# Optimization experiments

Hardware: AMD Instinct MI355X
Metric: run time of the kernel (lower is better)

The kernel has to match this reference:

```python
import jax, jax.numpy as jnp
import numpy as np

B, S, D = 512, 199, 128
PRO, SKILL = 20000, 500


def setup_inputs() -> dict:
    key = jax.random.key(0)
    ks = jax.random.split(key, 32)
    rn = lambda k, shape: jax.random.normal(k, shape, dtype=jnp.float32) * 0.05
    inp = {}
    inp["last_problem"] = jax.random.randint(ks[0], (B, S), 0, PRO, dtype=jnp.int32)
    inp["last_skill"] = jax.random.randint(ks[1], (B, S), 0, SKILL, dtype=jnp.int32)
    inp["last_ans"] = jax.random.randint(ks[2], (B, S), 0, 2, dtype=jnp.int32)
    inp["next_problem"] = jax.random.randint(ks[3], (B, S), 0, PRO, dtype=jnp.int32)
    inp["next_skill"] = jax.random.randint(ks[4], (B, S), 0, SKILL, dtype=jnp.int32)
    inp["next_ans"] = jax.random.randint(ks[5], (B, S), 0, 2, dtype=jnp.int32)
    inp["pro_embed"] = rn(ks[6], (PRO, D))
    inp["skill_embed"] = rn(ks[7], (SKILL, D))
    inp["ans_embed"] = rn(ks[8], (2, D))
    inp["time_embed"] = rn(ks[9], (200, D))
    inp["ls_state"] = rn(ks[10], (1, D))
    inp["pro_state0"] = rn(ks[11], (199, D))
    inp["skill_state0"] = rn(ks[12], (199, D))
    inp["akt_pro_diff"] = rn(ks[13], (PRO, 1))
    inp["akt_pro_change"] = rn(ks[14], (SKILL, D))
    # Linear weights stored as [in, out] (torch W.T); biases zero-init.
    inp["W_pf"] = rn(ks[15], (2 * D, D)); inp["b_pf"] = jnp.zeros((D,), jnp.float32)
    inp["W_sf"] = rn(ks[16], (2 * D, D)); inp["b_sf"] = jnp.zeros((D,), jnp.float32)
    inp["W_af"] = rn(ks[17], (2 * D, D)); inp["b_af"] = jnp.zeros((D,), jnp.float32)
    inp["W_ps"] = rn(ks[18], (2 * D, D)); inp["b_ps"] = jnp.zeros((D,), jnp.float32)
    inp["W_ss"] = rn(ks[19], (2 * D, D)); inp["b_ss"] = jnp.zeros((D,), jnp.float32)
    inp["W_as"] = rn(ks[20], (2 * D, D)); inp["b_as"] = jnp.zeros((D,), jnp.float32)
    inp["W_o1"] = rn(ks[21], (4 * D, D)); inp["b_o1"] = jnp.zeros((D,), jnp.float32)
    inp["W_o2"] = rn(ks[22], (D, 1));     inp["b_o2"] = jnp.zeros((1,), jnp.float32)
    return inp


def _forward(next_problem, next_skill, next_ans,
             pro_embed, skill_embed, ans_embed, time_embed, ls_state,
             pro_state0, skill_state0, akt_pro_diff, akt_pro_change,
             W_pf, b_pf, W_sf, b_sf, W_af, b_af,
             W_ps, b_ps, W_ss, b_ss, W_as, b_as,
             W_o1, b_o1, W_o2, b_o2):
    Bb, Ss = next_problem.shape
    Dd = pro_embed.shape[1]
    # [B,S,D] question embedding with AKT-style difficulty modulation
    npe = (pro_embed[next_problem] + skill_embed[next_skill]
           + akt_pro_diff[next_problem] * akt_pro_change[next_skill])
    nX = npe + ans_embed[next_ans]
    atge = time_embed[1]  # all_time_gap == 1 every step
    bidx = jnp.arange(Bb)

    def step(carry, x):
        pro_state, skill_state, all_state, lpt_tab, lst_tab = carry
        t, npe_t, nX_t, pidx, sidx = x
        # gather last-seen states via per-batch time indices
        lpt = lpt_tab[bidx, pidx]               # [B] int
        lbp = pro_state[bidx, lpt]              # [B,D]
        tge = time_embed[t - lpt]               # [B,D]
        lst = lst_tab[bidx, sidx]
        lbs = skill_state[bidx, lst]
        stge = time_embed[t - lst]
        # forget gates
        lbp = lbp * jax.nn.sigmoid(jnp.concatenate([lbp, tge], -1) @ W_pf + b_pf)
        lbs = lbs * jax.nn.sigmoid(jnp.concatenate([lbs, stge], -1) @ W_sf + b_sf)
        atge_b = jnp.broadcast_to(atge, all_state.shape)
        la = all_state * jax.nn.sigmoid(jnp.concatenate([all_state, atge_b], -1) @ W_af + b_af)
        # prediction head
        final = jnp.concatenate([la, lbp, lbs, npe_t], -1)  # [B,4D]
        P = jax.nn.sigmoid(jax.nn.relu(final @ W_o1 + b_o1) @ W_o2 + b_o2)[:, 0]
        # state updates
        new_all = la + jnp.tanh(jnp.concatenate([la, nX_t], -1) @ W_as + b_as)
        new_pro = lbp + jnp.tanh(jnp.concatenate([lbp, nX_t], -1) @ W_ps + b_ps)
        new_skill = lbs + jnp.tanh(jnp.concatenate([lbs, nX_t], -1) @ W_ss + b_ss)
        # scatter time and state back
        lpt_tab = lpt_tab.at[bidx, pidx].set(t)
        lst_tab = lst_tab.at[bidx, sidx].set(t)
        pro_state = jax.lax.dynamic_update_slice_in_dim(pro_state, new_pro[:, None, :], t, axis=1)
        skill_state = jax.lax.dynamic_update_slice_in_dim(skill_state, new_skill[:, None, :], t, axis=1)
        return (pro_state, skill_state, new_all, lpt_tab, lst_tab), P

    init = (jnp.broadcast_to(pro_state0[None], (Bb, pro_state0.shape[0], Dd)),
            jnp.broadcast_to(skill_state0[None], (Bb, skill_state0.shape[0], Dd)),
            jnp.broadcast_to(ls_state, (Bb, Dd)),
            jnp.zeros((Bb, akt_pro_diff.shape[0]), jnp.int32),
            jnp.zeros((Bb, akt_pro_change.shape[0]), jnp.int32))
    xs = (jnp.arange(Ss, dtype=jnp.int32),
          jnp.swapaxes(npe, 0, 1), jnp.swapaxes(nX, 0, 1),
          next_problem.T, next_skill.T)
    _, Ps = jax.lax.scan(step, init, xs)  # Ps: [S,B]
    return Ps.T  # [B,S]


def reference(last_problem, last_skill, last_ans, next_problem, next_skill, next_ans,
              pro_embed, skill_embed, ans_embed, time_embed, ls_state,
              pro_state0, skill_state0, akt_pro_diff, akt_pro_change,
              W_pf, b_pf, W_sf, b_sf, W_af, b_af,
              W_ps, b_ps, W_ss, b_ss, W_as, b_as,
              W_o1, b_o1, W_o2, b_o2):
    # last_problem/last_skill/last_ans are only used for shape in the original forward
    return _forward(next_problem, next_skill, next_ans,
                    pro_embed, skill_embed, ans_embed, time_embed, ls_state,
                    pro_state0, skill_state0, akt_pro_diff, akt_pro_change,
                    W_pf, b_pf, W_sf, b_sf, W_af, b_af,
                    W_ps, b_ps, W_ss, b_ss, W_as, b_as,
                    W_o1, b_o1, W_o2, b_o2)
```

## Files before the change

kernel.cpp:

```cpp
#include <hip/hip_runtime.h>
#include <hip/hip_bf16.h>

typedef __bf16 bf16;
typedef bf16 bf16x8 __attribute__((ext_vector_type(8)));
typedef bf16 bf16x4 __attribute__((ext_vector_type(4)));
typedef float f32x4 __attribute__((ext_vector_type(4)));
typedef unsigned int u32;
typedef unsigned short u16;

#define Bsz 512
#define Ssz 199
#define Dsz 128
#define GR 16
#define NBLK (Bsz / GR)
#define BTot (Bsz * Ssz)

__device__ __forceinline__ float fsig(float x) {
  return __builtin_amdgcn_rcpf(1.f + __builtin_amdgcn_exp2f(x * -1.44269504f));
}
__device__ __forceinline__ float ftanh(float x) {
  return 1.f - 2.f * __builtin_amdgcn_rcpf(1.f + __builtin_amdgcn_exp2f(x * 2.88539008f));
}
__device__ __forceinline__ f32x4 mfma16(bf16x8 a, bf16x8 b, f32x4 c) {
  return __builtin_amdgcn_mfma_f32_16x16x32_bf16(a, b, c, 0, 0, 0);
}
__device__ __forceinline__ bf16x8 ldfrag(const bf16* PW, int KS, int nt, int ks, int lane) {
  return *(const bf16x8*)&PW[(size_t)((nt * KS + ks) * 64 + lane) * 8];
}
__device__ __forceinline__ void keep(bf16x8& v) {
  f32x4& f = reinterpret_cast<f32x4&>(v);
  asm volatile("" : "+v"(f));
}
__device__ __forceinline__ void barL() {
  __builtin_amdgcn_sched_barrier(0);
  asm volatile("s_waitcnt lgkmcnt(0)" ::: "memory");
  __builtin_amdgcn_s_barrier();
  __builtin_amdgcn_sched_barrier(0);
}

__global__ void k_idx(const int* __restrict__ np_, const int* __restrict__ ns_,
                      const int* __restrict__ na_, u32* __restrict__ idx) {
  __shared__ u16 tabP[20000];
  __shared__ u16 tabS[500];
  __shared__ u16 pb[Ssz], sb[Ssz];
  __shared__ unsigned char ab[Ssz];
  int b = blockIdx.x;
  for (int i = threadIdx.x; i < 20000; i += blockDim.x) tabP[i] = 0;
  for (int i = threadIdx.x; i < 500; i += blockDim.x) tabS[i] = 0;
  for (int i = threadIdx.x; i < Ssz; i += blockDim.x) {
    pb[i] = (u16)np_[b * Ssz + i];
    sb[i] = (u16)ns_[b * Ssz + i];
    ab[i] = (unsigned char)na_[b * Ssz + i];
  }
  __syncthreads();
  if (threadIdx.x == 0) {
    for (int t = 0; t < Ssz; ++t) {
      int p = pb[t], s = sb[t];
      idx[b * Ssz + t] = (u32)tabP[p] | ((u32)tabS[s] << 8) | ((u32)ab[t] << 16);
      tabP[p] = (u16)t;
      tabS[s] = (u16)t;
    }
  }
}

__global__ void k_pack(const float* __restrict__ W, bf16* __restrict__ dst, int K) {
  int g = blockIdx.x * blockDim.x + threadIdx.x;
  int KS = K / 32;
  int total = 8 * KS * 64;
  if (g >= total) return;
  int l = g & 63;
  int ks = (g >> 6) % KS;
  int nt = (g >> 6) / KS;
  int col = nt * 16 + (l & 15);
  int k0 = ks * 32 + (l >> 4) * 8;
  bf16x8 v;
  for (int j = 0; j < 8; ++j) v[j] = (bf16)W[(size_t)(k0 + j) * 128 + col];
  *(bf16x8*)&dst[(size_t)g * 8] = v;
}

__global__ void k_tge(const float* __restrict__ TE, const float* __restrict__ W,
                      const float* __restrict__ bias, float* __restrict__ dst) {
  __shared__ float te[128];
  int d = blockIdx.x, n = threadIdx.x;
  te[n] = TE[d * 128 + n];
  __syncthreads();
  float acc = bias[n];
  for (int k = 0; k < 128; ++k) acc += te[k] * W[(size_t)(128 + k) * 128 + n];
  dst[d * 128 + n] = acc;
}

__global__ void k_embed(const int* __restrict__ np_, const int* __restrict__ ns_,
                        const float* __restrict__ pe, const float* __restrict__ se,
                        const float* __restrict__ diff, const float* __restrict__ chg,
                        bf16* __restrict__ npe) {
  int g = blockIdx.x * 256 + threadIdx.x;
  int bt = g >> 5, cg = (g & 31) * 4;
  if (bt >= BTot) return;
  int p = np_[bt], s = ns_[bt];
  float d = diff[p];
  f32x4 a = *(const f32x4*)&pe[(size_t)p * 128 + cg];
  f32x4 b = *(const f32x4*)&se[(size_t)s * 128 + cg];
  f32x4 c = *(const f32x4*)&chg[(size_t)s * 128 + cg];
  bf16x4 v;
  for (int j = 0; j < 4; ++j) v[j] = (bf16)(a[j] + b[j] + d * c[j]);
  *(bf16x4*)&npe[(size_t)bt * 128 + cg] = v;
}

struct MainParams {
  const int *next_problem, *next_skill;
  const float *pro_embed, *skill_embed, *akt_pro_diff, *akt_pro_change;
  const float *ans_embed;
  const float *ls_state, *pro_state0, *skill_state0;
  const u32 *idx;
  const bf16 *npe;
  const float *TGEp, *TGEs, *cAF;
  const bf16 *PWpf, *PWsf, *PWaf, *PWps, *PWss, *PWas;
  const float *b_ps, *b_ss, *b_as;
  bf16 *proSt, *skSt, *Sla, *Slbp, *Slbs;
};

template <int EMB>
__global__ void __launch_bounds__(512, 1) k_main(MainParams P) {
  const int b0 = blockIdx.x * GR;
  const int tid = threadIdx.x;
  const int lane = tid & 63;
  const int wv = tid >> 6;
  const int r32 = tid >> 5;
  const int c4 = (tid & 31) * 4;
  const int arow = lane & 15, apos = (lane >> 4) * 8;
  const int rb = (lane >> 4) * 4;
  const int cA = wv * 16 + (lane & 15);

  __shared__ __align__(16) bf16 Ala[16][136], Albp[16][136], Albs[16][136], AnX[16][136];
  __shared__ __align__(16) bf16 STG0[16][132], STG1[16][132], STGa[16][132];
  __shared__ u32 idxL[GR * Ssz];

  bf16x8 Wpf[4], Wsf[4], Waf[4], Wps[8], Wss[8], Was[8];
#pragma unroll
  for (int ks = 0; ks < 4; ++ks) {
    Wpf[ks] = ldfrag(P.PWpf, 4, wv, ks, lane);
    Wsf[ks] = ldfrag(P.PWsf, 4, wv, ks, lane);
    Waf[ks] = ldfrag(P.PWaf, 4, wv, ks, lane);
  }
#pragma unroll
  for (int ks = 0; ks < 8; ++ks) {
    Wps[ks] = ldfrag(P.PWps, 8, wv, ks, lane);
    Wss[ks] = ldfrag(P.PWss, 8, wv, ks, lane);
    Was[ks] = ldfrag(P.PWas, 8, wv, ks, lane);
  }
#pragma unroll
  for (int ks = 0; ks < 4; ++ks) {
    keep(Wpf[ks]);
    keep(Wsf[ks]);
    keep(Waf[ks]);
  }
#pragma unroll
  for (int ks = 0; ks < 8; ++ks) {
    keep(Wps[ks]);
    keep(Wss[ks]);
    keep(Was[ks]);
  }
  const float bpsv = P.b_ps[cA], bssv = P.b_ss[cA], basv = P.b_as[cA], cafv = P.cAF[cA];
  float aeL[4], aeH[4];
#pragma unroll
  for (int j = 0; j < 4; ++j) {
    aeL[j] = P.ans_embed[c4 + j];
    aeH[j] = P.ans_embed[128 + c4 + j];
  }

  for (int i = tid; i < GR * Ssz; i += 512) idxL[i] = P.idx[b0 * Ssz + i];
  __syncthreads();

  float gpc[4], gsc[4];
  {
    bf16x4 va, vp, vs;
    for (int j = 0; j < 4; ++j) {
      va[j] = (bf16)P.ls_state[c4 + j];
      vp[j] = (bf16)P.pro_state0[c4 + j];
      vs[j] = (bf16)P.skill_state0[c4 + j];
    }
    *(bf16x4*)&Ala[r32][c4] = va;
    *(bf16x4*)&Albp[r32][c4] = vp;
    *(bf16x4*)&Albs[r32][c4] = vs;
    u32 iw0 = idxL[r32 * Ssz];
    int na0 = (iw0 >> 16) & 1;
    f32x4 np0;
    if (EMB) {
      bf16x4 nb = *(const bf16x4*)&P.npe[((size_t)(b0 + r32) * Ssz) * Dsz + c4];
      for (int j = 0; j < 4; ++j) np0[j] = (float)nb[j];
    } else {
      int bt = (b0 + r32) * Ssz;
      int np = P.next_problem[bt], ns = P.next_skill[bt];
      float d = P.akt_pro_diff[np];
      f32x4 a = *(const f32x4*)&P.pro_embed[(size_t)np * 128 + c4];
      f32x4 b = *(const f32x4*)&P.skill_embed[(size_t)ns * 128 + c4];
      f32x4 c = *(const f32x4*)&P.akt_pro_change[(size_t)ns * 128 + c4];
      for (int j = 0; j < 4; ++j) np0[j] = a[j] + b[j] + d * c[j];
    }
    bf16x4 vx;
    for (int j = 0; j < 4; ++j) vx[j] = (bf16)(np0[j] + (na0 ? aeH[j] : aeL[j]));
    *(bf16x4*)&AnX[r32][c4] = vx;
#pragma unroll
    for (int r = 0; r < 4; ++r) {
      gpc[r] = P.TGEp[cA];
      gsc[r] = P.TGEs[cA];
    }
  }
  __syncthreads();

  for (int t = 0; t < Ssz; ++t) {
    const bool pf = (t + 1 < Ssz);
    float gpn[4], gsn[4];
    bf16x4 pPro{}, pSk{}, pNp{};
    f32x4 pNpF{};
    u32 iwN = 0;
    if (pf) {
#pragma unroll
      for (int r = 0; r < 4; ++r) {
        u32 iw = idxL[(rb + r) * Ssz + t + 1];
        int lp = iw & 255, ls = (iw >> 8) & 255;
        gpn[r] = P.TGEp[(size_t)(t + 1 - lp) * Dsz + cA];
        gsn[r] = P.TGEs[(size_t)(t + 1 - ls) * Dsz + cA];
      }
      iwN = idxL[r32 * Ssz + t + 1];
      int lpN = iwN & 255, lsN = (iwN >> 8) & 255;
      if (lpN != t)
        pPro = *(const bf16x4*)&P.proSt[((size_t)(b0 + r32) * Ssz + lpN) * Dsz + c4];
      if (lsN != t)
        pSk = *(const bf16x4*)&P.skSt[((size_t)(b0 + r32) * Ssz + lsN) * Dsz + c4];
      if (EMB) {
        pNp = *(const bf16x4*)&P.npe[((size_t)(b0 + r32) * Ssz + t + 1) * Dsz + c4];
      } else {
        int bt = (b0 + r32) * Ssz + t + 1;
        int np = P.next_problem[bt], ns = P.next_skill[bt];
        float d = P.akt_pro_diff[np];
        f32x4 a = *(const f32x4*)&P.pro_embed[(size_t)np * 128 + c4];
        f32x4 b = *(const f32x4*)&P.skill_embed[(size_t)ns * 128 + c4];
        f32x4 c = *(const f32x4*)&P.akt_pro_change[(size_t)ns * 128 + c4];
        for (int j = 0; j < 4; ++j) pNpF[j] = a[j] + b[j] + d * c[j];
      }
    }
    f32x4 dpf{}, dsf{}, daf{};
#pragma unroll
    for (int ks = 0; ks < 4; ++ks) {
      bf16x8 ap = *(const bf16x8*)&Albp[arow][ks * 32 + apos];
      bf16x8 av = *(const bf16x8*)&Albs[arow][ks * 32 + apos];
      bf16x8 aa = *(const bf16x8*)&Ala[arow][ks * 32 + apos];
      dpf = mfma16(ap, Wpf[ks], dpf);
      dsf = mfma16(av, Wsf[ks], dsf);
      daf = mfma16(aa, Waf[ks], daf);
    }
    barL();
    float gP[4], gS[4], gA[4];
#pragma unroll
    for (int r = 0; r < 4; ++r) {
      int row = rb + r;
      float sp = (float)Albp[row][cA];
      float gv = sp * fsig(dpf[r] + gpc[r]);
      gP[r] = gv;
      Albp[row][cA] = (bf16)gv;
      float ss = (float)Albs[row][cA];
      float gw = ss * fsig(dsf[r] + gsc[r]);
      gS[r] = gw;
      Albs[row][cA] = (bf16)gw;
      float sa = (float)Ala[row][cA];
      float gx = sa * fsig(daf[r] + cafv);
      gA[r] = gx;
      Ala[row][cA] = (bf16)gx;
    }
    barL();
    f32x4 uas{}, ups{}, uss{};
#pragma unroll
    for (int ks = 0; ks < 4; ++ks) {
      bf16x8 aa = *(const bf16x8*)&Ala[arow][ks * 32 + apos];
      bf16x8 ap = *(const bf16x8*)&Albp[arow][ks * 32 + apos];
      bf16x8 av = *(const bf16x8*)&Albs[arow][ks * 32 + apos];
      bf16x8 ax = *(const bf16x8*)&AnX[arow][ks * 32 + apos];
      uas = mfma16(aa, Was[ks], uas);
      uas = mfma16(ax, Was[ks + 4], uas);
      ups = mfma16(ap, Wps[ks], ups);
      ups = mfma16(ax, Wps[ks + 4], ups);
      uss = mfma16(av, Wss[ks], uss);
      uss = mfma16(ax, Wss[ks + 4], uss);
    }
#pragma unroll
    for (int r = 0; r < 4; ++r) {
      int row = rb + r;
      STG0[row][cA] = (bf16)(gP[r] + ftanh(ups[r] + bpsv));
      STG1[row][cA] = (bf16)(gS[r] + ftanh(uss[r] + bssv));
      STGa[row][cA] = (bf16)(gA[r] + ftanh(uas[r] + basv));
    }
    barL();
    {
      size_t base = ((size_t)(b0 + r32) * Ssz + t) * Dsz + c4;
      *(bf16x4*)&P.Sla[base] = *(const bf16x4*)&Ala[r32][c4];
      *(bf16x4*)&P.Slbp[base] = *(const bf16x4*)&Albp[r32][c4];
      *(bf16x4*)&P.Slbs[base] = *(const bf16x4*)&Albs[r32][c4];
      bf16x4 npv = *(const bf16x4*)&STG0[r32][c4];
      bf16x4 nsv = *(const bf16x4*)&STG1[r32][c4];
      *(bf16x4*)&P.proSt[base] = npv;
      *(bf16x4*)&P.skSt[base] = nsv;
      if (pf) {
        int lpN = iwN & 255, lsN = (iwN >> 8) & 255, naN = (iwN >> 16) & 1;
        *(bf16x4*)&Ala[r32][c4] = *(const bf16x4*)&STGa[r32][c4];
        *(bf16x4*)&Albp[r32][c4] = (lpN == t) ? npv : pPro;
        *(bf16x4*)&Albs[r32][c4] = (lsN == t) ? nsv : pSk;
        bf16x4 vx;
        for (int j = 0; j < 4; ++j) {
          float f = EMB ? (float)pNp[j] : pNpF[j];
          vx[j] = (bf16)(f + (naN ? aeH[j] : aeL[j]));
        }
        *(bf16x4*)&AnX[r32][c4] = vx;
#pragma unroll
        for (int r = 0; r < 4; ++r) {
          gpc[r] = gpn[r];
          gsc[r] = gsn[r];
        }
      }
    }
    __syncthreads();
  }
}

struct HeadParams {
  const bf16 *Sla, *Slbp, *Slbs, *PWo1, *npe;
  const int *next_problem, *next_skill;
  const float *pro_embed, *skill_embed, *akt_pro_diff, *akt_pro_change;
  const float *b_o1, *W_o2, *b_o2;
  float *out;
};

template <int EMB>
__global__ void k_head(HeadParams P) {
  const int bt0 = blockIdx.x * 16;
  const int tid = threadIdx.x, lane = tid & 63, wv = tid >> 6;
  const int r16 = tid >> 4, c8 = (tid & 15) * 8;
  const int arow = lane & 15, apos = (lane >> 4) * 8;
  const int rb = (lane >> 4) * 4;
  const int nt0 = wv, nt1 = wv + 4;
  const int cAh = nt0 * 16 + (lane & 15), cBh = nt1 * 16 + (lane & 15);
  __shared__ __align__(16) bf16 Af[16][520];
  __shared__ float Hh[16][132];
  __shared__ float Hpart[16][16];
  __shared__ float w2s[128];
  if (tid < 128) w2s[tid] = P.W_o2[tid];
  {
    int bt = bt0 + r16;
    *(bf16x8*)&Af[r16][c8] = *(const bf16x8*)&P.Sla[(size_t)bt * 128 + c8];
    *(bf16x8*)&Af[r16][128 + c8] = *(const bf16x8*)&P.Slbp[(size_t)bt * 128 + c8];
    *(bf16x8*)&Af[r16][256 + c8] = *(const bf16x8*)&P.Slbs[(size_t)bt * 128 + c8];
    if (EMB) {
      *(bf16x8*)&Af[r16][384 + c8] = *(const bf16x8*)&P.npe[(size_t)bt * 128 + c8];
    } else {
      int np = P.next_problem[bt], ns = P.next_skill[bt];
      float diff = P.akt_pro_diff[np];
      f32x4 p0 = *(const f32x4*)&P.pro_embed[(size_t)np * 128 + c8];
      f32x4 p1 = *(const f32x4*)&P.pro_embed[(size_t)np * 128 + c8 + 4];
      f32x4 s0 = *(const f32x4*)&P.skill_embed[(size_t)ns * 128 + c8];
      f32x4 s1 = *(const f32x4*)&P.skill_embed[(size_t)ns * 128 + c8 + 4];
      f32x4 c0 = *(const f32x4*)&P.akt_pro_change[(size_t)ns * 128 + c8];
      f32x4 c1 = *(const f32x4*)&P.akt_pro_change[(size_t)ns * 128 + c8 + 4];
      bf16x8 vn;
      for (int j = 0; j < 4; ++j) {
        vn[j] = (bf16)(p0[j] + s0[j] + diff * c0[j]);
        vn[j + 4] = (bf16)(p1[j] + s1[j] + diff * c1[j]);
      }
      *(bf16x8*)&Af[r16][384 + c8] = vn;
    }
  }
  __syncthreads();
  f32x4 h0{}, h1{};
#pragma unroll
  for (int ks = 0; ks < 16; ++ks) {
    bf16x8 a = *(const bf16x8*)&Af[arow][ks * 32 + apos];
    h0 = mfma16(a, ldfrag(P.PWo1, 16, nt0, ks, lane), h0);
    h1 = mfma16(a, ldfrag(P.PWo1, 16, nt1, ks, lane), h1);
  }
  const float bo1A = P.b_o1[cAh], bo1B = P.b_o1[cBh];
  for (int r = 0; r < 4; ++r) {
    Hh[rb + r][cAh] = fmaxf(h0[r] + bo1A, 0.f);
    Hh[rb + r][cBh] = fmaxf(h1[r] + bo1B, 0.f);
  }
  __syncthreads();
  {
    int row = tid >> 4, cg = tid & 15;
    float s = 0.f;
    for (int j = 0; j < 8; ++j) s += Hh[row][cg * 8 + j] * w2s[cg * 8 + j];
    Hpart[row][cg] = s;
  }
  __syncthreads();
  if (tid < 16) {
    float s = 0.f;
    for (int k = 0; k < 16; ++k) s += Hpart[tid][k];
    P.out[bt0 + tid] = fsig(s + P.b_o2[0]);
  }
}

extern "C" void kernel_launch(void* const* d_in, const int* in_sizes, int n_in,
                              void* d_out, int out_size, void* d_ws, size_t ws_size,
                              hipStream_t stream) {
  const int* next_problem = (const int*)d_in[3];
  const int* next_skill = (const int*)d_in[4];
  const int* next_ans = (const int*)d_in[5];
  const float* pro_embed = (const float*)d_in[6];
  const float* skill_embed = (const float*)d_in[7];
  const float* ans_embed = (const float*)d_in[8];
  const float* time_embed = (const float*)d_in[9];
  const float* ls_state = (const float*)d_in[10];
  const float* pro_state0 = (const float*)d_in[11];
  const float* skill_state0 = (const float*)d_in[12];
  const float* akt_pro_diff = (const float*)d_in[13];
  const float* akt_pro_change = (const float*)d_in[14];
  const float* W_pf = (const float*)d_in[15];
  const float* b_pf = (const float*)d_in[16];
  const float* W_sf = (const float*)d_in[17];
  const float* b_sf = (const float*)d_in[18];
  const float* W_af = (const float*)d_in[19];
  const float* b_af = (const float*)d_in[20];
  const float* W_ps = (const float*)d_in[21];
  const float* b_ps = (const float*)d_in[22];
  const float* W_ss = (const float*)d_in[23];
  const float* b_ss = (const float*)d_in[24];
  const float* W_as = (const float*)d_in[25];
  const float* b_as = (const float*)d_in[26];
  const float* W_o1 = (const float*)d_in[27];
  const float* b_o1 = (const float*)d_in[28];
  const float* W_o2 = (const float*)d_in[29];
  const float* b_o2 = (const float*)d_in[30];

  char* ws = (char*)d_ws;
  size_t off = 0;
  auto alloc = [&](size_t bytes) -> void* {
    void* p = ws + off;
    off += bytes;
    off = (off + 255) & ~(size_t)255;
    return p;
  };
  bf16* proSt = (bf16*)alloc((size_t)Bsz * Ssz * Dsz * 2);
  bf16* skSt = (bf16*)alloc((size_t)Bsz * Ssz * Dsz * 2);
  u32* idx = (u32*)alloc((size_t)BTot * 4);
  float* TGEp = (float*)alloc(200 * 128 * 4);
  float* TGEs = (float*)alloc(200 * 128 * 4);
  float* cAF = (float*)alloc(128 * 4);
  bf16* PWpf = (bf16*)alloc(128 * 128 * 2);
  bf16* PWsf = (bf16*)alloc(128 * 128 * 2);
  bf16* PWaf = (bf16*)alloc(128 * 128 * 2);
  bf16* PWps = (bf16*)alloc(256 * 128 * 2);
  bf16* PWss = (bf16*)alloc(256 * 128 * 2);
  bf16* PWas = (bf16*)alloc(256 * 128 * 2);
  bf16* PWo1 = (bf16*)alloc(512 * 128 * 2);
  bf16* Sla = (bf16*)alloc((size_t)BTot * Dsz * 2);
  bf16* Slbp = (bf16*)alloc((size_t)BTot * Dsz * 2);
  bf16* Slbs = (bf16*)alloc((size_t)BTot * Dsz * 2);
  size_t off_base = off;
  bf16* npe = (bf16*)alloc((size_t)BTot * Dsz * 2);
  size_t off_emb = off;

  bool emb = (off_emb <= ws_size);
  if (!emb && off_base > ws_size) {
    hipMemsetAsync(d_out, 0xFF, (size_t)out_size * 4, stream);
    return;
  }

  k_idx<<<Bsz, 256, 0, stream>>>(next_problem, next_skill, next_ans, idx);
  k_pack<<<8, 256, 0, stream>>>(W_pf, PWpf, 128);
  k_pack<<<8, 256, 0, stream>>>(W_sf, PWsf, 128);
  k_pack<<<8, 256, 0, stream>>>(W_af, PWaf, 128);
  k_pack<<<16, 256, 0, stream>>>(W_ps, PWps, 256);
  k_pack<<<16, 256, 0, stream>>>(W_ss, PWss, 256);
  k_pack<<<16, 256, 0, stream>>>(W_as, PWas, 256);
  k_pack<<<32, 256, 0, stream>>>(W_o1, PWo1, 512);
  k_tge<<<200, 128, 0, stream>>>(time_embed, W_pf, b_pf, TGEp);
  k_tge<<<200, 128, 0, stream>>>(time_embed, W_sf, b_sf, TGEs);
  k_tge<<<1, 128, 0, stream>>>(time_embed + 128, W_af, b_af, cAF);
  if (emb)
    k_embed<<<(BTot * 32 + 255) / 256, 256, 0, stream>>>(
        next_problem, next_skill, pro_embed, skill_embed, akt_pro_diff, akt_pro_change, npe);

  MainParams mp;
  mp.next_problem = next_problem; mp.next_skill = next_skill;
  mp.pro_embed = pro_embed; mp.skill_embed = skill_embed;
  mp.akt_pro_diff = akt_pro_diff; mp.akt_pro_change = akt_pro_change;
  mp.ans_embed = ans_embed;
  mp.ls_state = ls_state; mp.pro_state0 = pro_state0; mp.skill_state0 = skill_state0;
  mp.idx = idx; mp.npe = npe;
  mp.TGEp = TGEp; mp.TGEs = TGEs; mp.cAF = cAF;
  mp.PWpf = PWpf; mp.PWsf = PWsf; mp.PWaf = PWaf;
  mp.PWps = PWps; mp.PWss = PWss; mp.PWas = PWas;
  mp.b_ps = b_ps; mp.b_ss = b_ss; mp.b_as = b_as;
  mp.proSt = proSt; mp.skSt = skSt;
  mp.Sla = Sla; mp.Slbp = Slbp; mp.Slbs = Slbs;

  HeadParams hp;
  hp.Sla = Sla; hp.Slbp = Slbp; hp.Slbs = Slbs; hp.PWo1 = PWo1; hp.npe = npe;
  hp.next_problem = next_problem; hp.next_skill = next_skill;
  hp.pro_embed = pro_embed; hp.skill_embed = skill_embed;
  hp.akt_pro_diff = akt_pro_diff; hp.akt_pro_change = akt_pro_change;
  hp.b_o1 = b_o1; hp.W_o2 = W_o2; hp.b_o2 = b_o2;
  hp.out = (float*)d_out;

  if (emb) {
    k_main<1><<<NBLK, 512, 0, stream>>>(mp);
    k_head<1><<<BTot / 16, 256, 0, stream>>>(hp);
  } else {
    k_main<0><<<NBLK, 512, 0, stream>>>(mp);
    k_head<0><<<BTot / 16, 256, 0, stream>>>(hp);
  }
}
```

Before: 691.5 us.

## Fuse output head into recurrent kernel and pre-gather time-gap and embedding tensors

The output MLP head (W_o1 matmul, ReLU, W_o2 dot, sigmoid) now runs inside the recurrent scan kernel on state already held in LDS. This removes the separate head kernel and the Sla/Slbp/Slbs round-trip through global memory. Embedding-plus-answer and time-gap gate terms are precomputed into time-major bf16 buffers by new kernels, so the loop does coalesced contiguous loads. State writeback is deferred one step with double-buffered staging. The cost is more registers (O1 fragments) and extra precompute bandwidth. There is also a new bf16 rounding of the time-gap terms.

```diff
diff --git a/kernel.cpp b/kernel.cpp
--- a/kernel.cpp
+++ b/kernel.cpp
@@ -31,32 +31,36 @@
   f32x4& f = reinterpret_cast<f32x4&>(v);
   asm volatile("" : "+v"(f));
 }
-__device__ __forceinline__ void barL() {
+__device__ __forceinline__ void barRaw() {
   __builtin_amdgcn_sched_barrier(0);
   asm volatile("s_waitcnt lgkmcnt(0)" ::: "memory");
   __builtin_amdgcn_s_barrier();
   __builtin_amdgcn_sched_barrier(0);
 }
+__device__ __forceinline__ void barVm() {
+  __builtin_amdgcn_sched_barrier(0);
+  asm volatile("s_waitcnt vmcnt(0) lgkmcnt(0)" ::: "memory");
+  __builtin_amdgcn_s_barrier();
+  __builtin_amdgcn_sched_barrier(0);
+}
 
 __global__ void k_idx(const int* __restrict__ np_, const int* __restrict__ ns_,
-                      const int* __restrict__ na_, u32* __restrict__ idx) {
+                      u32* __restrict__ idx) {
   __shared__ u16 tabP[20000];
   __shared__ u16 tabS[500];
   __shared__ u16 pb[Ssz], sb[Ssz];
-  __shared__ unsigned char ab[Ssz];
   int b = blockIdx.x;
   for (int i = threadIdx.x; i < 20000; i += blockDim.x) tabP[i] = 0;
   for (int i = threadIdx.x; i < 500; i += blockDim.x) tabS[i] = 0;
   for (int i = threadIdx.x; i < Ssz; i += blockDim.x) {
     pb[i] = (u16)np_[b * Ssz + i];
     sb[i] = (u16)ns_[b * Ssz + i];
-    ab[i] = (unsigned char)na_[b * Ssz + i];
   }
   __syncthreads();
   if (threadIdx.x == 0) {
     for (int t = 0; t < Ssz; ++t) {
       int p = pb[t], s = sb[t];
-      idx[b * Ssz + t] = (u32)tabP[p] | ((u32)tabS[s] << 8) | ((u32)ab[t] << 16);
+      idx[b * Ssz + t] = (u32)tabP[p] | ((u32)tabS[s] << 8);
       tabP[p] = (u16)t;
       tabS[s] = (u16)t;
     }
@@ -90,37 +94,66 @@
 }
 
 __global__ void k_embed(const int* __restrict__ np_, const int* __restrict__ ns_,
+                        const int* __restrict__ na_,
                         const float* __restrict__ pe, const float* __restrict__ se,
                         const float* __restrict__ diff, const float* __restrict__ chg,
-                        bf16* __restrict__ npe) {
+                        const float* __restrict__ ae,
+                        bf16* __restrict__ npeS, bf16* __restrict__ nXsS) {
   int g = blockIdx.x * 256 + threadIdx.x;
   int bt = g >> 5, cg = (g & 31) * 4;
   if (bt >= BTot) return;
-  int p = np_[bt], s = ns_[bt];
+  int b = bt / Ssz, t = bt - b * Ssz;
+  int p = np_[bt], s = ns_[bt], a = na_[bt];
   float d = diff[p];
-  f32x4 a = *(const f32x4*)&pe[(size_t)p * 128 + cg];
-  f32x4 b = *(const f32x4*)&se[(size_t)s * 128 + cg];
-  f32x4 c = *(const f32x4*)&chg[(size_t)s * 128 + cg];
-  bf16x4 v;
-  for (int j = 0; j < 4; ++j) v[j] = (bf16)(a[j] + b[j] + d * c[j]);
-  *(bf16x4*)&npe[(size_t)bt * 128 + cg] = v;
+  f32x4 vp = *(const f32x4*)&pe[(size_t)p * 128 + cg];
+  f32x4 vs = *(const f32x4*)&se[(size_t)s * 128 + cg];
+  f32x4 vc = *(const f32x4*)&chg[(size_t)s * 128 + cg];
+  f32x4 va = *(const f32x4*)&ae[(size_t)a * 128 + cg];
+  bf16x4 on, ox;
+  for (int j = 0; j < 4; ++j) {
+    float f = vp[j] + vs[j] + d * vc[j];
+    on[j] = (bf16)f;
+    ox[j] = (bf16)(f + va[j]);
+  }
+  size_t o = ((size_t)t * Bsz + b) * 128 + cg;
+  *(bf16x4*)&npeS[o] = on;
+  *(bf16x4*)&nXsS[o] = ox;
+}
+
+__global__ void k_tgb(const u32* __restrict__ idx, const float* __restrict__ TP,
+                      const float* __restrict__ TS, bf16* __restrict__ TGBp,
+                      bf16* __restrict__ TGBs) {
+  int g = blockIdx.x * 256 + threadIdx.x;
+  int bt = g >> 5, cg = (g & 31) * 4;
+  if (bt >= BTot) return;
+  int b = bt / Ssz, t = bt - b * Ssz;
+  u32 iw = idx[bt];
+  int dp = t - (int)(iw & 255);
+  int ds = t - (int)((iw >> 8) & 255);
+  f32x4 vp = *(const f32x4*)&TP[(size_t)dp * 128 + cg];
+  f32x4 vs = *(const f32x4*)&TS[(size_t)ds * 128 + cg];
+  bf16x4 op, os;
+  for (int j = 0; j < 4; ++j) {
+    op[j] = (bf16)vp[j];
+    os[j] = (bf16)vs[j];
+  }
+  size_t o = ((size_t)t * Bsz + b) * 128 + cg;
+  *(bf16x4*)&TGBp[o] = op;
+  *(bf16x4*)&TGBs[o] = os;
 }
 
 struct MainParams {
-  const int *next_problem, *next_skill;
-  const float *pro_embed, *skill_embed, *akt_pro_diff, *akt_pro_change;
-  const float *ans_embed;
   const float *ls_state, *pro_state0, *skill_state0;
   const u32 *idx;
-  const bf16 *npe;
-  const float *TGEp, *TGEs, *cAF;
-  const bf16 *PWpf, *PWsf, *PWaf, *PWps, *PWss, *PWas;
-  const float *b_ps, *b_ss, *b_as;
-  bf16 *proSt, *skSt, *Sla, *Slbp, *Slbs;
+  const bf16 *npeS, *nXsS, *TGBp, *TGBs;
+  const float *cAF;
+  const bf16 *PWpf, *PWsf, *PWaf, *PWps, *PWss, *PWas, *PWo1;
+  const float *b_ps, *b_ss, *b_as, *b_o1, *W_o2, *b_o2;
+  bf16 *proSt, *skSt;
+  float *out;
 };
 
-template <int EMB>
-__global__ void __launch_bounds__(512, 1) k_main(MainParams P) {
+__global__ void __launch_bounds__(512, 2) k_main(MainParams P) {
   const int b0 = blockIdx.x * GR;
   const int tid = threadIdx.x;
   const int lane = tid & 63;
@@ -131,16 +164,20 @@
   const int rb = (lane >> 4) * 4;
   const int cA = wv * 16 + (lane & 15);
 
-  __shared__ __align__(16) bf16 Ala[16][136], Albp[16][136], Albs[16][136], AnX[16][136];
-  __shared__ __align__(16) bf16 STG0[16][132], STG1[16][132], STGa[16][132];
+  __shared__ __align__(16) bf16 Ala[16][132], Albp[16][132], Albs[16][132];
+  __shared__ __align__(16) bf16 AnX[16][132], Anpe[16][132];
+  __shared__ __align__(16) bf16 STG0[2][16][132], STG1[2][16][132], STGa[16][132];
+  __shared__ float Hh[16][132];
+  __shared__ float Hpart[16][17];
+  __shared__ float w2s[128];
   __shared__ u32 idxL[GR * Ssz];
 
-  bf16x8 Wpf[4], Wsf[4], Waf[4], Wps[8], Wss[8], Was[8];
+  bf16x8 Gpf[4], Gsf[4], Gaf[4], Wps[8], Wss[8], Was[8], O1[16];
 #pragma unroll
   for (int ks = 0; ks < 4; ++ks) {
-    Wpf[ks] = ldfrag(P.PWpf, 4, wv, ks, lane);
-    Wsf[ks] = ldfrag(P.PWsf, 4, wv, ks, lane);
-    Waf[ks] = ldfrag(P.PWaf, 4, wv, ks, lane);
+    Gpf[ks] = ldfrag(P.PWpf, 4, wv, ks, lane);
+    Gsf[ks] = ldfrag(P.PWsf, 4, wv, ks, lane);
+    Gaf[ks] = ldfrag(P.PWaf, 4, wv, ks, lane);
   }
 #pragma unroll
   for (int ks = 0; ks < 8; ++ks) {
@@ -149,29 +186,20 @@
     Was[ks] = ldfrag(P.PWas, 8, wv, ks, lane);
   }
 #pragma unroll
-  for (int ks = 0; ks < 4; ++ks) {
-    keep(Wpf[ks]);
-    keep(Wsf[ks]);
-    keep(Waf[ks]);
-  }
-#pragma unroll
   for (int ks = 0; ks < 8; ++ks) {
     keep(Wps[ks]);
     keep(Wss[ks]);
     keep(Was[ks]);
   }
-  const float bpsv = P.b_ps[cA], bssv = P.b_ss[cA], basv = P.b_as[cA], cafv = P.cAF[cA];
-  float aeL[4], aeH[4];
-#pragma unroll
-  for (int j = 0; j < 4; ++j) {
-    aeL[j] = P.ans_embed[c4 + j];
-    aeH[j] = P.ans_embed[128 + c4 + j];
-  }
+#pragma unroll
+  for (int ks = 0; ks < 16; ++ks) O1[ks] = ldfrag(P.PWo1, 16, wv, ks, lane);
+
+  const float bpsv = P.b_ps[cA], bssv = P.b_ss[cA], basv = P.b_as[cA];
+  const float cafv = P.cAF[cA], bo1v = P.b_o1[cA], bo2 = P.b_o2[0];
+  if (tid < 128) w2s[tid] = P.W_o2[tid];
 
   for (int i = tid; i < GR * Ssz; i += 512) idxL[i] = P.idx[b0 * Ssz + i];
-  __syncthreads();
-
-  float gpc[4], gsc[4];
+
   {
     bf16x4 va, vp, vs;
     for (int j = 0; j < 4; ++j) {
@@ -182,62 +210,52 @@
     *(bf16x4*)&Ala[r32][c4] = va;
     *(bf16x4*)&Albp[r32][c4] = vp;
     *(bf16x4*)&Albs[r32][c4] = vs;
-    u32 iw0 = idxL[r32 * Ssz];
-    int na0 = (iw0 >> 16) & 1;
-    f32x4 np0;
-    if (EMB) {
-      bf16x4 nb = *(const bf16x4*)&P.npe[((size_t)(b0 + r32) * Ssz) * Dsz + c4];
-      for (int j = 0; j < 4; ++j) np0[j] = (float)nb[j];
-    } else {
-      int bt = (b0 + r32) * Ssz;
-      int np = P.next_problem[bt], ns = P.next_skill[bt];
-      float d = P.akt_pro_diff[np];
-      f32x4 a = *(const f32x4*)&P.pro_embed[(size_t)np * 128 + c4];
-      f32x4 b = *(const f32x4*)&P.skill_embed[(size_t)ns * 128 + c4];
-      f32x4 c = *(const f32x4*)&P.akt_pro_change[(size_t)ns * 128 + c4];
-      for (int j = 0; j < 4; ++j) np0[j] = a[j] + b[j] + d * c[j];
-    }
-    bf16x4 vx;
-    for (int j = 0; j < 4; ++j) vx[j] = (bf16)(np0[j] + (na0 ? aeH[j] : aeL[j]));
-    *(bf16x4*)&AnX[r32][c4] = vx;
-#pragma unroll
-    for (int r = 0; r < 4; ++r) {
-      gpc[r] = P.TGEp[cA];
-      gsc[r] = P.TGEs[cA];
-    }
+    size_t so = (size_t)(b0 + r32) * Dsz + c4;
+    *(bf16x4*)&Anpe[r32][c4] = *(const bf16x4*)&P.npeS[so];
+    *(bf16x4*)&AnX[r32][c4] = *(const bf16x4*)&P.nXsS[so];
+  }
+  bf16 gpcP[4], gpcS[4];
+#pragma unroll
+  for (int r = 0; r < 4; ++r) {
+    size_t go = (size_t)(b0 + rb + r) * Dsz + cA;
+    gpcP[r] = P.TGBp[go];
+    gpcS[r] = P.TGBs[go];
   }
   __syncthreads();
 
   for (int t = 0; t < Ssz; ++t) {
     const bool pf = (t + 1 < Ssz);
-    float gpn[4], gsn[4];
-    bf16x4 pPro{}, pSk{}, pNp{};
-    f32x4 pNpF{};
-    u32 iwN = 0;
+    const int cur = t & 1, prv = cur ^ 1;
+    if (t > 0) {
+      size_t sb = ((size_t)(b0 + r32) * Ssz + (t - 1)) * Dsz + c4;
+      *(bf16x4*)&P.proSt[sb] = *(const bf16x4*)&STG0[prv][r32][c4];
+      *(bf16x4*)&P.skSt[sb] = *(const bf16x4*)&STG1[prv][r32][c4];
+      if (tid < 16) {
+        float s = 0.f;
+#pragma unroll
+        for (int k = 0; k < 16; ++k) s += Hpart[tid][k];
+        P.out[(size_t)(b0 + tid) * Ssz + (t - 1)] = fsig(s + bo2);
+      }
+    }
+    int lpN = 0, lsN = 0;
+    bf16x4 pPro{}, pSk{}, pNpe{}, pNxs{};
+    bf16 gpnP[4], gpnS[4];
     if (pf) {
+      u32 iw = idxL[r32 * Ssz + t + 1];
+      lpN = iw & 255;
+      lsN = (iw >> 8) & 255;
+      if (lpN < t - 1)
+        pPro = *(const bf16x4*)&P.proSt[((size_t)(b0 + r32) * Ssz + lpN) * Dsz + c4];
+      if (lsN < t - 1)
+        pSk = *(const bf16x4*)&P.skSt[((size_t)(b0 + r32) * Ssz + lsN) * Dsz + c4];
+      size_t so = ((size_t)(t + 1) * Bsz + (b0 + r32)) * Dsz + c4;
+      pNpe = *(const bf16x4*)&P.npeS[so];
+      pNxs = *(const bf16x4*)&P.nXsS[so];
 #pragma unroll
       for (int r = 0; r < 4; ++r) {
-        u32 iw = idxL[(rb + r) * Ssz + t + 1];
-        int lp = iw & 255, ls = (iw >> 8) & 255;
-        gpn[r] = P.TGEp[(size_t)(t + 1 - lp) * Dsz + cA];
-        gsn[r] = P.TGEs[(size_t)(t + 1 - ls) * Dsz + cA];
-      }
-      iwN = idxL[r32 * Ssz + t + 1];
-      int lpN = iwN & 255, lsN = (iwN >> 8) & 255;
-      if (lpN != t)
-        pPro = *(const bf16x4*)&P.proSt[((size_t)(b0 + r32) * Ssz + lpN) * Dsz + c4];
-      if (lsN != t)
-        pSk = *(const bf16x4*)&P.skSt[((size_t)(b0 + r32) * Ssz + lsN) * Dsz + c4];
-      if (EMB) {
-        pNp = *(const bf16x4*)&P.npe[((size_t)(b0 + r32) * Ssz + t + 1) * Dsz + c4];
-      } else {
-        int bt = (b0 + r32) * Ssz + t + 1;
-        int np = P.next_problem[bt], ns = P.next_skill[bt];
-        float d = P.akt_pro_diff[np];
-        f32x4 a = *(const f32x4*)&P.pro_embed[(size_t)np * 128 + c4];
-        f32x4 b = *(const f32x4*)&P.skill_embed[(size_t)ns * 128 + c4];
-        f32x4 c = *(const f32x4*)&P.akt_pro_change[(size_t)ns * 128 + c4];
-        for (int j = 0; j < 4; ++j) pNpF[j] = a[j] + b[j] + d * c[j];
+        size_t go = ((size_t)(t + 1) * Bsz + (b0 + rb + r)) * Dsz + cA;
+        gpnP[r] = P.TGBp[go];
+        gpnS[r] = P.TGBs[go];
       }
     }
     f32x4 dpf{}, dsf{}, daf{};
@@ -246,153 +264,86 @@
       bf16x8 ap = *(const bf16x8*)&Albp[arow][ks * 32 + apos];
       bf16x8 av = *(const bf16x8*)&Albs[arow][ks * 32 + apos];
       bf16x8 aa = *(const bf16x8*)&Ala[arow][ks * 32 + apos];
-      dpf = mfma16(ap, Wpf[ks], dpf);
-      dsf = mfma16(av, Wsf[ks], dsf);
-      daf = mfma16(aa, Waf[ks], daf);
-    }
-    barL();
+      dpf = mfma16(ap, Gpf[ks], dpf);
+      dsf = mfma16(av, Gsf[ks], dsf);
+      daf = mfma16(aa, Gaf[ks], daf);
+    }
+    barRaw();
     float gP[4], gS[4], gA[4];
 #pragma unroll
     for (int r = 0; r < 4; ++r) {
       int row = rb + r;
-      float sp = (float)Albp[row][cA];
-      float gv = sp * fsig(dpf[r] + gpc[r]);
+      float gv = (float)Albp[row][cA] * fsig(dpf[r] + (float)gpcP[r]);
       gP[r] = gv;
       Albp[row][cA] = (bf16)gv;
-      float ss = (float)Albs[row][cA];
-      float gw = ss * fsig(dsf[r] + gsc[r]);
+      float gw = (float)Albs[row][cA] * fsig(dsf[r] + (float)gpcS[r]);
       gS[r] = gw;
       Albs[row][cA] = (bf16)gw;
-      float sa = (float)Ala[row][cA];
-      float gx = sa * fsig(daf[r] + cafv);
+      float gx = (float)Ala[row][cA] * fsig(daf[r] + cafv);
       gA[r] = gx;
       Ala[row][cA] = (bf16)gx;
     }
-    barL();
-    f32x4 uas{}, ups{}, uss{};
+    barRaw();
+    f32x4 uas{}, ups{}, uss{}, hh{};
 #pragma unroll
     for (int ks = 0; ks < 4; ++ks) {
       bf16x8 aa = *(const bf16x8*)&Ala[arow][ks * 32 + apos];
       bf16x8 ap = *(const bf16x8*)&Albp[arow][ks * 32 + apos];
       bf16x8 av = *(const bf16x8*)&Albs[arow][ks * 32 + apos];
       bf16x8 ax = *(const bf16x8*)&AnX[arow][ks * 32 + apos];
+      bf16x8 an = *(const bf16x8*)&Anpe[arow][ks * 32 + apos];
       uas = mfma16(aa, Was[ks], uas);
       uas = mfma16(ax, Was[ks + 4], uas);
       ups = mfma16(ap, Wps[ks], ups);
       ups = mfma16(ax, Wps[ks + 4], ups);
       uss = mfma16(av, Wss[ks], uss);
       uss = mfma16(ax, Wss[ks + 4], uss);
+      hh = mfma16(aa, O1[ks], hh);
+      hh = mfma16(ap, O1[ks + 4], hh);
+      hh = mfma16(av, O1[ks + 8], hh);
+      hh = mfma16(an, O1[ks + 12], hh);
     }
 #pragma unroll
     for (int r = 0; r < 4; ++r) {
       int row = rb + r;
-      STG0[row][cA] = (bf16)(gP[r] + ftanh(ups[r] + bpsv));
-      STG1[row][cA] = (bf16)(gS[r] + ftanh(uss[r] + bssv));
       STGa[row][cA] = (bf16)(gA[r] + ftanh(uas[r] + basv));
-    }
-    barL();
-    {
-      size_t base = ((size_t)(b0 + r32) * Ssz + t) * Dsz + c4;
-      *(bf16x4*)&P.Sla[base] = *(const bf16x4*)&Ala[r32][c4];
-      *(bf16x4*)&P.Slbp[base] = *(const bf16x4*)&Albp[r32][c4];
-      *(bf16x4*)&P.Slbs[base] = *(const bf16x4*)&Albs[r32][c4];
-      bf16x4 npv = *(const bf16x4*)&STG0[r32][c4];
-      bf16x4 nsv = *(const bf16x4*)&STG1[r32][c4];
-      *(bf16x4*)&P.proSt[base] = npv;
-      *(bf16x4*)&P.skSt[base] = nsv;
-      if (pf) {
-        int lpN = iwN & 255, lsN = (iwN >> 8) & 255, naN = (iwN >> 16) & 1;
-        *(bf16x4*)&Ala[r32][c4] = *(const bf16x4*)&STGa[r32][c4];
-        *(bf16x4*)&Albp[r32][c4] = (lpN == t) ? npv : pPro;
-        *(bf16x4*)&Albs[r32][c4] = (lsN == t) ? nsv : pSk;
-        bf16x4 vx;
-        for (int j = 0; j < 4; ++j) {
-          float f = EMB ? (float)pNp[j] : pNpF[j];
-          vx[j] = (bf16)(f + (naN ? aeH[j] : aeL[j]));
-        }
-        *(bf16x4*)&AnX[r32][c4] = vx;
-#pragma unroll
-        for (int r = 0; r < 4; ++r) {
-          gpc[r] = gpn[r];
-          gsc[r] = gsn[r];
-        }
+      STG0[cur][row][cA] = (bf16)(gP[r] + ftanh(ups[r] + bpsv));
+      STG1[cur][row][cA] = (bf16)(gS[r] + ftanh(uss[r] + bssv));
+      Hh[row][cA] = fmaxf(hh[r] + bo1v, 0.f);
+    }
+    barVm();
+    if (tid < 256) {
+      int row = tid >> 4, cg = tid & 15;
+      float s = 0.f;
+#pragma unroll
+      for (int j = 0; j < 8; ++j) s += Hh[row][cg * 8 + j] * w2s[cg * 8 + j];
+      Hpart[row][cg] = s;
+    }
+    if (pf) {
+      *(bf16x4*)&Ala[r32][c4] = *(const bf16x4*)&STGa[r32][c4];
+      bf16x4 scur = *(const bf16x4*)&STG0[cur][r32][c4];
+      bf16x4 sprv = *(const bf16x4*)&STG0[prv][r32][c4];
+      bf16x4 bp = (lpN == t) ? scur : ((lpN == t - 1) ? sprv : pPro);
+      *(bf16x4*)&Albp[r32][c4] = bp;
+      scur = *(const bf16x4*)&STG1[cur][r32][c4];
+      sprv = *(const bf16x4*)&STG1[prv][r32][c4];
+      bf16x4 bs = (lsN == t) ? scur : ((lsN == t - 1) ? sprv : pSk);
+      *(bf16x4*)&Albs[r32][c4] = bs;
+      *(bf16x4*)&AnX[r32][c4] = pNxs;
+      *(bf16x4*)&Anpe[r32][c4] = pNpe;
+#pragma unroll
+      for (int r = 0; r < 4; ++r) {
+        gpcP[r] = gpnP[r];
+        gpcS[r] = gpnS[r];
       }
     }
-    __syncthreads();
-  }
-}
-
-struct HeadParams {
-  const bf16 *Sla, *Slbp, *Slbs, *PWo1, *npe;
-  const int *next_problem, *next_skill;
-  const float *pro_embed, *skill_embed, *akt_pro_diff, *akt_pro_change;
-  const float *b_o1, *W_o2, *b_o2;
-  float *out;
-};
-
-template <int EMB>
-__global__ void k_head(HeadParams P) {
-  const int bt0 = blockIdx.x * 16;
-  const int tid = threadIdx.x, lane = tid & 63, wv = tid >> 6;
-  const int r16 = tid >> 4, c8 = (tid & 15) * 8;
-  const int arow = lane & 15, apos = (lane >> 4) * 8;
-  const int rb = (lane >> 4) * 4;
-  const int nt0 = wv, nt1 = wv + 4;
-  const int cAh = nt0 * 16 + (lane & 15), cBh = nt1 * 16 + (lane & 15);
-  __shared__ __align__(16) bf16 Af[16][520];
-  __shared__ float Hh[16][132];
-  __shared__ float Hpart[16][16];
-  __shared__ float w2s[128];
-  if (tid < 128) w2s[tid] = P.W_o2[tid];
-  {
-    int bt = bt0 + r16;
-    *(bf16x8*)&Af[r16][c8] = *(const bf16x8*)&P.Sla[(size_t)bt * 128 + c8];
-    *(bf16x8*)&Af[r16][128 + c8] = *(const bf16x8*)&P.Slbp[(size_t)bt * 128 + c8];
-    *(bf16x8*)&Af[r16][256 + c8] = *(const bf16x8*)&P.Slbs[(size_t)bt * 128 + c8];
-    if (EMB) {
-      *(bf16x8*)&Af[r16][384 + c8] = *(const bf16x8*)&P.npe[(size_t)bt * 128 + c8];
-    } else {
-      int np = P.next_problem[bt], ns = P.next_skill[bt];
-      float diff = P.akt_pro_diff[np];
-      f32x4 p0 = *(const f32x4*)&P.pro_embed[(size_t)np * 128 + c8];
-      f32x4 p1 = *(const f32x4*)&P.pro_embed[(size_t)np * 128 + c8 + 4];
-      f32x4 s0 = *(const f32x4*)&P.skill_embed[(size_t)ns * 128 + c8];
-      f32x4 s1 = *(const f32x4*)&P.skill_embed[(size_t)ns * 128 + c8 + 4];
-      f32x4 c0 = *(const f32x4*)&P.akt_pro_change[(size_t)ns * 128 + c8];
-      f32x4 c1 = *(const f32x4*)&P.akt_pro_change[(size_t)ns * 128 + c8 + 4];
-      bf16x8 vn;
-      for (int j = 0; j < 4; ++j) {
-        vn[j] = (bf16)(p0[j] + s0[j] + diff * c0[j]);
-        vn[j + 4] = (bf16)(p1[j] + s1[j] + diff * c1[j]);
-      }
-      *(bf16x8*)&Af[r16][384 + c8] = vn;
-    }
-  }
-  __syncthreads();
-  f32x4 h0{}, h1{};
-#pragma unroll
-  for (int ks = 0; ks < 16; ++ks) {
-    bf16x8 a = *(const bf16x8*)&Af[arow][ks * 32 + apos];
-    h0 = mfma16(a, ldfrag(P.PWo1, 16, nt0, ks, lane), h0);
-    h1 = mfma16(a, ldfrag(P.PWo1, 16, nt1, ks, lane), h1);
-  }
-  const float bo1A = P.b_o1[cAh], bo1B = P.b_o1[cBh];
-  for (int r = 0; r < 4; ++r) {
-    Hh[rb + r][cAh] = fmaxf(h0[r] + bo1A, 0.f);
-    Hh[rb + r][cBh] = fmaxf(h1[r] + bo1B, 0.f);
-  }
-  __syncthreads();
-  {
-    int row = tid >> 4, cg = tid & 15;
-    float s = 0.f;
-    for (int j = 0; j < 8; ++j) s += Hh[row][cg * 8 + j] * w2s[cg * 8 + j];
-    Hpart[row][cg] = s;
-  }
-  __syncthreads();
+    barRaw();
+  }
   if (tid < 16) {
     float s = 0.f;
+#pragma unroll
     for (int k = 0; k < 16; ++k) s += Hpart[tid][k];
-    P.out[bt0 + tid] = fsig(s + P.b_o2[0]);
+    P.out[(size_t)(b0 + tid) * Ssz + (Ssz - 1)] = fsig(s + bo2);
   }
 }
 
@@ -449,20 +400,17 @@
   bf16* PWss = (bf16*)alloc(256 * 128 * 2);
   bf16* PWas = (bf16*)alloc(256 * 128 * 2);
   bf16* PWo1 = (bf16*)alloc(512 * 128 * 2);
-  bf16* Sla = (bf16*)alloc((size_t)BTot * Dsz * 2);
-  bf16* Slbp = (bf16*)alloc((size_t)BTot * Dsz * 2);
-  bf16* Slbs = (bf16*)alloc((size_t)BTot * Dsz * 2);
-  size_t off_base = off;
-  bf16* npe = (bf16*)alloc((size_t)BTot * Dsz * 2);
-  size_t off_emb = off;
-
-  bool emb = (off_emb <= ws_size);
-  if (!emb && off_base > ws_size) {
+  bf16* npeS = (bf16*)alloc((size_t)BTot * Dsz * 2);
+  bf16* nXsS = (bf16*)alloc((size_t)BTot * Dsz * 2);
+  bf16* TGBp = (bf16*)alloc((size_t)BTot * Dsz * 2);
+  bf16* TGBs = (bf16*)alloc((size_t)BTot * Dsz * 2);
+
+  if (off > ws_size) {
     hipMemsetAsync(d_out, 0xFF, (size_t)out_size * 4, stream);
     return;
   }
 
-  k_idx<<<Bsz, 256, 0, stream>>>(next_problem, next_skill, next_ans, idx);
+  k_idx<<<Bsz, 256, 0, stream>>>(next_problem, next_skill, idx);
   k_pack<<<8, 256, 0, stream>>>(W_pf, PWpf, 128);
   k_pack<<<8, 256, 0, stream>>>(W_sf, PWsf, 128);
   k_pack<<<8, 256, 0, stream>>>(W_af, PWaf, 128);
@@ -473,37 +421,22 @@
   k_tge<<<200, 128, 0, stream>>>(time_embed, W_pf, b_pf, TGEp);
   k_tge<<<200, 128, 0, stream>>>(time_embed, W_sf, b_sf, TGEs);
   k_tge<<<1, 128, 0, stream>>>(time_embed + 128, W_af, b_af, cAF);
-  if (emb)
-    k_embed<<<(BTot * 32 + 255) / 256, 256, 0, stream>>>(
-        next_problem, next_skill, pro_embed, skill_embed, akt_pro_diff, akt_pro_change, npe);
+  k_embed<<<(BTot * 32 + 255) / 256, 256, 0, stream>>>(
+      next_problem, next_skill, next_ans, pro_embed, skill_embed, akt_pro_diff,
+      akt_pro_change, ans_embed, npeS, nXsS);
+  k_tgb<<<(BTot * 32 + 255) / 256, 256, 0, stream>>>(idx, TGEp, TGEs, TGBp, TGBs);
 
   MainParams mp;
-  mp.next_problem = next_problem; mp.next_skill = next_skill;
-  mp.pro_embed = pro_embed; mp.skill_embed = skill_embed;
-  mp.akt_pro_diff = akt_pro_diff; mp.akt_pro_change = akt_pro_change;
-  mp.ans_embed = ans_embed;
   mp.ls_state = ls_state; mp.pro_state0 = pro_state0; mp.skill_state0 = skill_state0;
-  mp.idx = idx; mp.npe = npe;
-  mp.TGEp = TGEp; mp.TGEs = TGEs; mp.cAF = cAF;
+  mp.idx = idx;
+  mp.npeS = npeS; mp.nXsS = nXsS; mp.TGBp = TGBp; mp.TGBs = TGBs;
+  mp.cAF = cAF;
   mp.PWpf = PWpf; mp.PWsf = PWsf; mp.PWaf = PWaf;
-  mp.PWps = PWps; mp.PWss = PWss; mp.PWas = PWas;
+  mp.PWps = PWps; mp.PWss = PWss; mp.PWas = PWas; mp.PWo1 = PWo1;
   mp.b_ps = b_ps; mp.b_ss = b_ss; mp.b_as = b_as;
+  mp.b_o1 = b_o1; mp.W_o2 = W_o2; mp.b_o2 = b_o2;
   mp.proSt = proSt; mp.skSt = skSt;
-  mp.Sla = Sla; mp.Slbp = Slbp; mp.Slbs = Slbs;
-
-  HeadParams hp;
-  hp.Sla = Sla; hp.Slbp = Slbp; hp.Slbs = Slbs; hp.PWo1 = PWo1; hp.npe = npe;
-  hp.next_problem = next_problem; hp.next_skill = next_skill;
-  hp.pro_embed = pro_embed; hp.skill_embed = skill_embed;
-  hp.akt_pro_diff = akt_pro_diff; hp.akt_pro_change = akt_pro_change;
-  hp.b_o1 = b_o1; hp.W_o2 = W_o2; hp.b_o2 = b_o2;
-  hp.out = (float*)d_out;
-
-  if (emb) {
-    k_main<1><<<NBLK, 512, 0, stream>>>(mp);
-    k_head<1><<<BTot / 16, 256, 0, stream>>>(hp);
-  } else {
-    k_main<0><<<NBLK, 512, 0, stream>>>(mp);
-    k_head<0><<<BTot / 16, 256, 0, stream>>>(hp);
-  }
-}
+  mp.out = (float*)d_out;
+
+  k_main<<<NBLK, 512, 0, stream>>>(mp);
+}
```

Result: slower. 1.655 ms (+139.3%).
